# Kernel optimization log

Hardware: AMD Instinct MI355X
Metric: run time of the kernel (lower is better)

## Reference

```python
import jax, jax.numpy as jnp
import numpy as np

STRIDES = (4, 8, 16, 32, 64, 128)
MAPS = (128, 64, 32, 16, 8, 4)
VAR0, VAR1 = 0.1, 0.2
CLS_TH, NMS_TH, FINAL_TH = 0.05, 0.3, 0.5


def _decode_scale(ocls, oreg, stride):
    # ocls: [1,2,H,W], oreg: [1,4,H,W] -> dets [H*W, 5] = (x1,y1,x2,y2,score)
    prob = jax.nn.softmax(ocls, axis=1)[0, 1]          # [H,W] face probability
    H, W = prob.shape
    s = jnp.float32(stride)
    pcx = s / 2 + jnp.arange(W, dtype=jnp.float32)[None, :] * s   # prior center x
    pcy = s / 2 + jnp.arange(H, dtype=jnp.float32)[:, None] * s   # prior center y
    pwh = s * 4.0                                                 # prior w = h = 4*stride
    loc = oreg[0]                                                 # [4,H,W]
    cx = pcx + loc[0] * VAR0 * pwh
    cy = pcy + loc[1] * VAR0 * pwh
    w = pwh * jnp.exp(loc[2] * VAR1)
    h = pwh * jnp.exp(loc[3] * VAR1)
    x1 = cx - w / 2
    y1 = cy - h / 2
    x2 = x1 + w
    y2 = y1 + h
    return jnp.stack([x1.ravel(), y1.ravel(), x2.ravel(), y2.ravel(), prob.ravel()], axis=1)


def _nms_keep(dets, valid):
    # Greedy NMS (torch-style, +1 box convention), fixed trip count, returns keep mask.
    N = dets.shape[0]
    scores = jnp.where(valid, dets[:, 4], -jnp.inf)
    order = jnp.argsort(-scores)            # descending by score, invalid last
    b = dets[order]
    v = valid[order]
    x1, y1, x2, y2 = b[:, 0], b[:, 1], b[:, 2], b[:, 3]
    areas = (x2 - x1 + 1.0) * (y2 - y1 + 1.0)
    pos = jnp.arange(N)

    def body(i, carry):
        sup, keep = carry
        active = jnp.logical_and(jnp.logical_not(sup[i]), v[i])
        keep = keep.at[i].set(active)
        xx1 = jnp.maximum(x1[i], x1)
        yy1 = jnp.maximum(y1[i], y1)
        xx2 = jnp.minimum(x2[i], x2)
        yy2 = jnp.minimum(y2[i], y2)
        w = jnp.maximum(xx2 - xx1 + 1.0, 0.0)
        h = jnp.maximum(yy2 - yy1 + 1.0, 0.0)
        inter = w * h
        iou = inter / (areas[i] + areas - inter)
        sup = sup | (active & (iou > NMS_TH) & (pos > i))
        return sup, keep

    sup0 = jnp.logical_not(v)
    _, keep_sorted = jax.lax.fori_loop(0, N, body, (sup0, jnp.zeros(N, dtype=bool)))
    return jnp.zeros(N, dtype=bool).at[order].set(keep_sorted)


def _forward(ol1, ol2, ol3, ol4, ol5, ol6, ol7, ol8, ol9, ol10, ol11, ol12):
    olist = [ol1, ol2, ol3, ol4, ol5, ol6, ol7, ol8, ol9, ol10, ol11, ol12]
    dets = jnp.concatenate(
        [_decode_scale(olist[2 * i], olist[2 * i + 1], STRIDES[i]) for i in range(6)],
        axis=0)                              # [N,5]
    valid = dets[:, 4] > CLS_TH              # threshold stage (score > 0.05)
    # NMS selection is index logic -> constant w.r.t. differentiation
    keep = _nms_keep(jax.lax.stop_gradient(dets), valid)
    final = keep & (dets[:, 4] > FINAL_TH)   # post-NMS score > 0.5 filter
    # fixed-shape equivalent of gathering kept rows: zero out non-kept rows
    return dets * final[:, None].astype(dets.dtype)


def setup_inputs() -> dict:
    key = jax.random.key(0)
    inp = {}
    for i, hw in enumerate(MAPS):
        kc, kr, key = jax.random.split(key, 3)
        inp[f"ol{2 * i + 1}"] = jax.random.normal(kc, (1, 2, hw, hw), dtype=jnp.float32)
        inp[f"ol{2 * i + 2}"] = jax.random.normal(kr, (1, 4, hw, hw), dtype=jnp.float32)
    return inp


def reference(ol1, ol2, ol3, ol4, ol5, ol6, ol7, ol8, ol9, ol10, ol11, ol12):
    return _forward(ol1, ol2, ol3, ol4, ol5, ol6, ol7, ol8, ol9, ol10, ol11, ol12)
```

## Files before the change

kernel.cpp:

```cpp
#include <hip/hip_runtime.h>
#include <stdint.h>

#define N_TOTAL 21840
#define NA      21888
#define W_MAX   342
#define TOT_ENT 3753792u
#define NMS_TH  0.3f
#define FINAL_TH 0.5f
#define NSLICE  8
#define SCAN_T  768
#define NPUSH   11
#define PLANES  704
#define GRP     4
#define NBAND   7
#define GMAX    86

struct Inputs { const float* cls[6]; const float* reg[6]; };

__device__ __forceinline__ void block_bar() {
  asm volatile("s_waitcnt lgkmcnt(0)\n\ts_barrier" ::: "memory");
}

__device__ __forceinline__ unsigned wbase_u(unsigned w) {
  return 64u * (342u * w - (w * (w - 1u)) / 2u);
}

__global__ void decode_kernel(Inputs in,
                              float* __restrict__ dx1, float* __restrict__ dy1,
                              float* __restrict__ dx2, float* __restrict__ dy2,
                              float* __restrict__ dsc,
                              unsigned long long* __restrict__ ckey,
                              unsigned int* __restrict__ Mc,
                              unsigned int* __restrict__ rank32,
                              unsigned int* __restrict__ wcnt,
                              float* __restrict__ out) {
#pragma clang fp contract(off)
  int gid = blockIdx.x * blockDim.x + threadIdx.x;
  if (gid >= N_TOTAL) return;

  rank32[gid] = 0u;
  wcnt[gid] = 0u;
  if (gid < NA - N_TOTAL) wcnt[N_TOTAL + gid] = 0u;

  int sc, local;
  if      (gid < 16384) { sc = 0; local = gid;         }
  else if (gid < 20480) { sc = 1; local = gid - 16384; }
  else if (gid < 21504) { sc = 2; local = gid - 20480; }
  else if (gid < 21760) { sc = 3; local = gid - 21504; }
  else if (gid < 21824) { sc = 4; local = gid - 21760; }
  else                  { sc = 5; local = gid - 21824; }

  const int Wd     = 128 >> sc;
  const int stride = 4 << sc;
  const int HW     = Wd * Wd;
  const int x = local & (Wd - 1);
  const int y = local >> (7 - sc);

  const float* cls = in.cls[sc];
  const float* reg = in.reg[sc];

  float c0 = cls[local];
  float c1 = cls[HW + local];
  float m  = fmaxf(c0, c1);
  float e0 = expf(c0 - m);
  float e1 = expf(c1 - m);
  float prob = e1 / (e0 + e1);

  float l0 = reg[local];
  float l1 = reg[HW + local];
  float l2 = reg[2 * HW + local];
  float l3 = reg[3 * HW + local];

  float sF  = (float)stride;
  float pcx = 0.5f * sF + (float)x * sF;
  float pcy = 0.5f * sF + (float)y * sF;
  float pwh = sF * 4.0f;

  float cx = pcx + ((l0 * 0.1f) * pwh);
  float cy = pcy + ((l1 * 0.1f) * pwh);
  float w  = pwh * expf(l2 * 0.2f);
  float h  = pwh * expf(l3 * 0.2f);
  float x1 = cx - w * 0.5f;
  float y1 = cy - h * 0.5f;
  float x2 = x1 + w;
  float y2 = y1 + h;

  dx1[gid] = x1; dy1[gid] = y1; dx2[gid] = x2; dy2[gid] = y2; dsc[gid] = prob;

  out[gid * 5 + 0] = 0.0f;
  out[gid * 5 + 1] = 0.0f;
  out[gid * 5 + 2] = 0.0f;
  out[gid * 5 + 3] = 0.0f;
  out[gid * 5 + 4] = 0.0f;

  if (prob > FINAL_TH) {
    unsigned int pos = atomicAdd(Mc, 1u);
    ckey[pos] = ((unsigned long long)__float_as_uint(prob) << 32) |
                (unsigned int)(~(unsigned int)gid);
  }
}

__global__ void __launch_bounds__(256)
rank_kernel(const unsigned long long* __restrict__ ckey,
            const unsigned int* __restrict__ Mc,
            const float* __restrict__ dx1, const float* __restrict__ dy1,
            const float* __restrict__ dx2, const float* __restrict__ dy2,
            float* __restrict__ sx1, float* __restrict__ sy1,
            float* __restrict__ sx2, float* __restrict__ sy2,
            unsigned int* __restrict__ sorig,
            unsigned int* __restrict__ rank32) {
  __shared__ unsigned long long tile[256];
  const unsigned int M = *Mc;
  if (blockIdx.x * 256u >= M) return;
  const int t = (int)threadIdx.x;
  const int p = (int)blockIdx.x * 256 + t;
  unsigned long long mykey = (p < (int)M) ? ckey[p] : 0ull;
  const int S  = (int)((M + NSLICE - 1) / NSLICE);
  const int lo = (int)blockIdx.y * S;
  const int hi = min((int)M, lo + S);
  int partial = 0;
  const int nt = (hi > lo) ? ((hi - lo + 255) >> 8) : 0;
  for (int ti = 0; ti < nt; ++ti) {
    int j = lo + ti * 256 + t;
    tile[t] = (j < hi) ? ckey[j] : 0ull;
    __syncthreads();
#pragma unroll 8
    for (int q = 0; q < 256; ++q) partial += (tile[q] > mykey) ? 1 : 0;
    __syncthreads();
  }
  if (p < (int)M) {
    unsigned int pack = (unsigned int)partial | (1u << 24);
    unsigned int old  = atomicAdd(&rank32[p], pack);
    unsigned int newv = old + pack;
    if ((newv >> 24) == NSLICE) {
      int r = (int)(newv & 0xFFFFFF);
      unsigned int orig = ~(unsigned int)(mykey & 0xffffffffull);
      sx1[r] = dx1[orig];
      sy1[r] = dy1[orig];
      sx2[r] = dx2[orig];
      sy2[r] = dy2[orig];
      sorig[r] = orig;
    }
  }
}

__global__ void __launch_bounds__(1024)
pairs_kernel(const float* __restrict__ sx1, const float* __restrict__ sy1,
             const float* __restrict__ sx2, const float* __restrict__ sy2,
             const unsigned int* __restrict__ Mc,
             unsigned long long* __restrict__ diag,
             unsigned long long* __restrict__ bandT,
             unsigned int* __restrict__ wcnt,
             unsigned short* __restrict__ rlMeta,
             unsigned long long* __restrict__ rlBits) {
#pragma clang fp contract(off)
  const int M = (int)*Mc;
  const int W = (M + 63) >> 6;
  const int rw = (int)blockIdx.y;
  const int cwg = (int)blockIdx.x << 4;
  if (rw >= W || cwg >= W || cwg + 22 < rw) return;

  const int t = (int)threadIdx.x;
  const int g = t >> 6, l = t & 63;
  const int cw = cwg + g;

  __shared__ float cx1[1024], cy1[1024], cx2[1024], cy2[1024], car[1024];
  __shared__ unsigned wvcnt[16], wvbase[16];
  {
    int c = (cw << 6) + l;
    if (cw < W && c < M) {
      float a = sx1[c], b = sy1[c], d = sx2[c], e = sy2[c];
      cx1[t] = a; cy1[t] = b; cx2[t] = d; cy2[t] = e;
      car[t] = (d - a + 1.0f) * (e - b + 1.0f);
    }
  }
  __syncthreads();

  const int rwg = rw >> 2, cg = cw >> 2;
  const bool inW    = (cw < W);
  const bool isDiag = inW && (cw == rw);
  const bool isBand = inW && (cw < rw) && (cg >= rwg - 1);
  const bool isCsr  = inW && (cg >= rwg + 2);
  const bool any    = isDiag || isBand || isCsr;

  const int r = (rw << 6) + l;
  unsigned long long bits = 0ull;
  if (any && r < M) {
    float ax1 = sx1[r], ay1 = sy1[r], ax2 = sx2[r], ay2 = sy2[r];
    float aarea = (ax2 - ax1 + 1.0f) * (ay2 - ay1 + 1.0f);
    const int cmax = min(64, M - (cw << 6));
    const int sb = g << 6;
    for (int cc = 0; cc < cmax; ++cc) {
      float xx1 = fmaxf(ax1, cx1[sb + cc]);
      float yy1 = fmaxf(ay1, cy1[sb + cc]);
      float xx2 = fminf(ax2, cx2[sb + cc]);
      float yy2 = fminf(ay2, cy2[sb + cc]);
      float ww = fmaxf(xx2 - xx1 + 1.0f, 0.0f);
      float hh = fmaxf(yy2 - yy1 + 1.0f, 0.0f);
      float inter = ww * hh;
      float iou = inter / (aarea + car[sb + cc] - inter);
      if (iou > NMS_TH) bits |= (1ull << cc);
    }
  }
  if (isDiag)      diag[r] = bits;
  else if (isBand) bandT[(size_t)(rw - cw - 1) * NA + r] = bits;

  unsigned long long ball = 0ull;
  unsigned myrank = 0u;
  {
    bool mine = isCsr && (bits != 0ull);
    ball = __ballot(mine);
    myrank = (unsigned)__popcll(ball & ((1ull << l) - 1ull));
    if (l == 0) wvcnt[g] = (unsigned)__popcll(ball);
  }
  __syncthreads();
  if (t == 0) {
    unsigned tot = 0u;
    unsigned pre[16];
#pragma unroll
    for (int i = 0; i < 16; ++i) { pre[i] = tot; tot += wvcnt[i]; }
    unsigned base = (tot != 0u) ? atomicAdd(&wcnt[rw], tot) : 0u;
#pragma unroll
    for (int i = 0; i < 16; ++i) wvbase[i] = base + pre[i];
  }
  __syncthreads();
  if (isCsr && bits != 0ull) {
    unsigned slot = wbase_u((unsigned)rw) + wvbase[g] + myrank;
    rlMeta[slot] = (unsigned short)(((unsigned)l << 9) | (unsigned)cw);
    rlBits[slot] = bits;
  }
}

__global__ void __launch_bounds__(SCAN_T)
scan_kernel(const unsigned long long* __restrict__ diag,
            const unsigned long long* __restrict__ bandT,
            const unsigned int* __restrict__ wcnt,
            const unsigned short* __restrict__ rlMeta,
            const unsigned long long* __restrict__ rlBits,
            const unsigned int* __restrict__ sorig,
            const unsigned int* __restrict__ Mc,
            const float* __restrict__ dx1, const float* __restrict__ dy1,
            const float* __restrict__ dx2, const float* __restrict__ dy2,
            const float* __restrict__ dsc,
            float* __restrict__ out) {
  __shared__ unsigned long long sup[W_MAX];
  __shared__ unsigned long long kmls[W_MAX];
  __shared__ unsigned lds_wcnt[W_MAX];
  __shared__ unsigned gdone[GMAX];
  __shared__ volatile unsigned sflag;
  const int t = (int)threadIdx.x;
  const int g = t >> 6, l = t & 63;
  const int M = (int)*Mc;
  const int W = (M + 63) >> 6;
  const int NS = (W + 3) >> 2;

  for (int i = t; i < W_MAX; i += SCAN_T) {
    sup[i] = 0ull; kmls[i] = 0ull; lds_wcnt[i] = wcnt[i];
  }
  for (int i = t; i < GMAX; i += SCAN_T) gdone[i] = 0u;
  if (t == 0) sflag = 0u;
  block_bar();

  if (g == 0) {
    __builtin_amdgcn_s_setprio(1);
    const unsigned long long lowm = (1ull << l) - 1ull;
    unsigned long long dc[4], dn[4];
    unsigned long long bc[4][NBAND], bn[4][NBAND];
    unsigned long long kp[4] = {0ull, 0ull, 0ull, 0ull};
#pragma unroll
    for (int i = 0; i < 4; ++i) {
      int v = i, vc = (v < W) ? v : 0;
      dc[i] = diag[(vc << 6) + l];
#pragma unroll
      for (int d = 1; d <= NBAND; ++d)
        if (d <= i + 4) bc[i][d - 1] = bandT[(size_t)(d - 1) * NA + (vc << 6) + l];
    }
#pragma unroll
    for (int i = 0; i < 4; ++i) {
      int v = 4 + i, vc = (v < W) ? v : 0;
      dn[i] = diag[(vc << 6) + l];
#pragma unroll
      for (int d = 1; d <= NBAND; ++d)
        if (d <= i + 4) bn[i][d - 1] = bandT[(size_t)(d - 1) * NA + (vc << 6) + l];
    }
    for (int s = 0; s < NS; ++s) {
      const int v0 = s << 2;
      unsigned long long accp[4];
#pragma unroll
      for (int i = 0; i < 4; ++i) {
        unsigned long long a = 0ull;
#pragma unroll
        for (int d = 1; d <= NBAND; ++d)
          if (d <= i + 4 && d > i) a |= (bc[i][d - 1] & kp[i - d + 4]);
        accp[i] = a;
      }
      if (s >= 2) {
        while (*(volatile unsigned*)&gdone[s - 2] < (unsigned)NPUSH) {}
        asm volatile("" ::: "memory");
      }
      unsigned long long sv[4];
#pragma unroll
      for (int i = 0; i < 4; ++i)
        sv[i] = (v0 + i < W) ? sup[v0 + i] : 0ull;
      unsigned long long kc[4];
#pragma unroll
      for (int i = 0; i < 4; ++i) {
        const int v = v0 + i;
        unsigned long long kept = 0ull;
        if (v < W) {
          unsigned long long acc = accp[i];
#pragma unroll
          for (int d = 1; d <= 3; ++d)
            if (d <= i) acc |= (bc[i][d - 1] & kc[i - d]);
          unsigned long long incoming = __ballot(acc != 0ull);
          const int n = min(64, M - (v << 6));
          unsigned long long wm = (n >= 64) ? ~0ull : ((1ull << n) - 1ull);
          unsigned long long pend = (~(sv[i] | incoming)) & wm;
          const unsigned long long dv = dc[i] & lowm;
          unsigned long long dead = ~pend, und = pend;
          while (und) {
            unsigned long long bS = __ballot((dv & kept) != 0ull) & und;
            unsigned long long bK = __ballot((dv & ~dead) == 0ull) & und;
            kept |= bK; dead |= bS; und &= ~(bK | bS);
          }
          if (l == i) kmls[v] = kept;
        }
        kc[i] = kept;
      }
      asm volatile("s_waitcnt lgkmcnt(0)" ::: "memory");
      if (l == 0) sflag = (unsigned)(s + 1);
#pragma unroll
      for (int i = 0; i < 4; ++i) kp[i] = kc[i];
#pragma unroll
      for (int i = 0; i < 4; ++i) {
        dc[i] = dn[i];
#pragma unroll
        for (int d = 0; d < NBAND; ++d)
          if (d <= i + 3) bc[i][d] = bn[i][d];
      }
      const int vn = v0 + 8;
#pragma unroll
      for (int i = 0; i < 4; ++i) {
        int v = vn + i, vc = (v < W) ? v : 0;
        dn[i] = diag[(vc << 6) + l];
#pragma unroll
        for (int d = 1; d <= NBAND; ++d)
          if (d <= i + 4) bn[i][d - 1] = bandT[(size_t)(d - 1) * NA + (vc << 6) + l];
      }
    }
    __builtin_amdgcn_s_setprio(0);
  } else {
    const int p = (g - 1) * 64 + l;

#define PUSH_LOAD(mX, bX, gs)                                               \
    {                                                                       \
      _Pragma("unroll")                                                     \
      for (int i = 0; i < 4; ++i) {                                         \
        int v = (gs) * 4 + i;                                               \
        unsigned vc = (v < W) ? (unsigned)v : 0u;                           \
        unsigned base = wbase_u(vc);                                        \
        unsigned i0 = base + (unsigned)p;   if (i0 >= TOT_ENT) i0 = 0u;     \
        unsigned i1 = i0 + (unsigned)PLANES; if (i1 >= TOT_ENT) i1 = 0u;    \
        mX[i][0] = (unsigned)rlMeta[i0]; bX[i][0] = rlBits[i0];             \
        mX[i][1] = (unsigned)rlMeta[i1]; bX[i][1] = rlBits[i1];             \
      }                                                                     \
    }

    unsigned mA[4][2], mB[4][2];
    unsigned long long bA[4][2], bB[4][2];
    PUSH_LOAD(mA, bA, 0)
    PUSH_LOAD(mB, bB, 1)
    for (int s = 0; s < NS; ++s) {
      while (sflag < (unsigned)(s + 1)) __builtin_amdgcn_s_sleep(1);
      asm volatile("" ::: "memory");
#pragma unroll
      for (int i = 0; i < 4; ++i) {
        const int v = (s << 2) + i;
        if (v < W) {
          const unsigned tw = lds_wcnt[v];
          const unsigned long long km = kmls[v];
          if (km != 0ull && tw != 0u) {
            if ((unsigned)p < tw && ((km >> (mA[i][0] >> 9)) & 1ull))
              atomicOr(&sup[mA[i][0] & 511u], bA[i][0]);
            if ((unsigned)p + (unsigned)PLANES < tw &&
                ((km >> (mA[i][1] >> 9)) & 1ull))
              atomicOr(&sup[mA[i][1] & 511u], bA[i][1]);
            if (tw > 2u * (unsigned)PLANES) {
              unsigned base = wbase_u((unsigned)v);
              for (unsigned ii = (unsigned)p + 2u * (unsigned)PLANES;
                   ii < tw; ii += (unsigned)PLANES) {
                unsigned sl = base + ii; if (sl >= TOT_ENT) sl = TOT_ENT - 1u;
                unsigned mm = (unsigned)rlMeta[sl];
                if ((km >> (mm >> 9)) & 1ull)
                  atomicOr(&sup[mm & 511u], rlBits[sl]);
              }
            }
          }
        }
      }
      asm volatile("s_waitcnt lgkmcnt(0)" ::: "memory");
      if (l == 0) atomicAdd(&gdone[s], 1u);
#pragma unroll
      for (int i = 0; i < 4; ++i) {
        mA[i][0] = mB[i][0]; mA[i][1] = mB[i][1];
        bA[i][0] = bB[i][0]; bA[i][1] = bB[i][1];
      }
      PUSH_LOAD(mB, bB, s + 2)
    }
#undef PUSH_LOAD
  }
  block_bar();

  for (int i = t; i < (W << 6); i += SCAN_T) {
    if ((kmls[i >> 6] >> (i & 63)) & 1ull) {
      unsigned int orig = sorig[i];
      out[(size_t)orig * 5 + 0] = dx1[orig];
      out[(size_t)orig * 5 + 1] = dy1[orig];
      out[(size_t)orig * 5 + 2] = dx2[orig];
      out[(size_t)orig * 5 + 3] = dy2[orig];
      out[(size_t)orig * 5 + 4] = dsc[orig];
    }
  }
}

__global__ void __launch_bounds__(1024)
nms_kernel(const float* __restrict__ sx1, const float* __restrict__ sy1,
           const float* __restrict__ sx2, const float* __restrict__ sy2,
           const unsigned int* __restrict__ sorig,
           const unsigned int* __restrict__ Mc,
           unsigned int* __restrict__ keepflag) {
#pragma clang fp contract(off)
  __shared__ unsigned long long sup[W_MAX];
  __shared__ unsigned long long inrow[64];
  __shared__ float wx1[64], wy1[64], wx2[64], wy2[64], warea[64];
  __shared__ unsigned long long keptmask_sh;

  const int t = (int)threadIdx.x;
  const int M = (int)*Mc;
  const int W = (M + 63) >> 6;

  for (int i = t; i < W_MAX; i += 1024) sup[i] = 0ull;
  __syncthreads();

  for (int w = 0; w < W; ++w) {
    const int base = w << 6;
    const int n = min(64, M - base);
    if (t < 64) {
      if (t < n) {
        float a = sx1[base + t], b = sy1[base + t];
        float c = sx2[base + t], d = sy2[base + t];
        wx1[t] = a; wy1[t] = b; wx2[t] = c; wy2[t] = d;
        warea[t] = (c - a + 1.0f) * (d - b + 1.0f);
      }
    } else if (t < 128) {
      inrow[t - 64] = 0ull;
    }
    __syncthreads();
    {
      int r = t & 63, seg = t >> 6;
      unsigned long long bits = 0ull;
      if (r < n) {
        float ax1 = wx1[r], ay1 = wy1[r], ax2 = wx2[r], ay2 = wy2[r];
        float aarea = warea[r];
        for (int c = seg * 4; c < seg * 4 + 4; ++c) {
          if (c > r && c < n) {
            float xx1 = fmaxf(ax1, wx1[c]);
            float yy1 = fmaxf(ay1, wy1[c]);
            float xx2 = fminf(ax2, wx2[c]);
            float yy2 = fminf(ay2, wy2[c]);
            float ww = fmaxf(xx2 - xx1 + 1.0f, 0.0f);
            float hh = fmaxf(yy2 - yy1 + 1.0f, 0.0f);
            float inter = ww * hh;
            float iou = inter / (aarea + warea[c] - inter);
            if (iou > NMS_TH) bits |= (1ull << c);
          }
        }
      }
      if (bits) atomicOr(&inrow[r], bits);
    }
    __syncthreads();
    if (t < 64) {
      unsigned long long wordmask = (n >= 64) ? ~0ull : ((1ull << n) - 1ull);
      unsigned long long pending = (~sup[w]) & wordmask;
      unsigned long long kept = 0ull;
      while (pending) {
        int i = __builtin_ctzll(pending);
        kept |= (1ull << i);
        pending &= ~(inrow[i] | (1ull << i));
      }
      if (t == 0) keptmask_sh = kept;
      if (t < n && ((kept >> t) & 1ull)) keepflag[sorig[base + t]] = 1u;
    }
    __syncthreads();
    unsigned long long km = keptmask_sh;
    if (km) {
      int wid = t >> 6, lane = t & 63;
      for (int jw = w + 1 + wid; (jw << 6) < M; jw += 16) {
        int j = (jw << 6) + lane;
        bool supj = false;
        if (j < M) {
          float jx1 = sx1[j], jy1 = sy1[j], jx2 = sx2[j], jy2 = sy2[j];
          float jarea = (jx2 - jx1 + 1.0f) * (jy2 - jy1 + 1.0f);
          unsigned long long mm = km;
          while (mm) {
            int r = __builtin_ctzll(mm);
            mm &= mm - 1ull;
            float xx1 = fmaxf(wx1[r], jx1);
            float yy1 = fmaxf(wy1[r], jy1);
            float xx2 = fminf(wx2[r], jx2);
            float yy2 = fminf(wy2[r], jy2);
            float ww = fmaxf(xx2 - xx1 + 1.0f, 0.0f);
            float hh = fmaxf(yy2 - yy1 + 1.0f, 0.0f);
            float inter = ww * hh;
            float iou = inter / (warea[r] + jarea - inter);
            if (iou > NMS_TH) { supj = true; break; }
          }
        }
        unsigned long long bal = __ballot(supj);
        if (lane == 0 && bal) atomicOr(&sup[jw], bal);
      }
    }
    __syncthreads();
  }
}

__global__ void output_kernel(const float* __restrict__ dx1, const float* __restrict__ dy1,
                              const float* __restrict__ dx2, const float* __restrict__ dy2,
                              const float* __restrict__ dsc,
                              const unsigned int* __restrict__ keepflag,
                              float* __restrict__ out) {
#pragma clang fp contract(off)
  int gid = blockIdx.x * blockDim.x + threadIdx.x;
  if (gid >= N_TOTAL) return;
  float f = keepflag[gid] ? 1.0f : 0.0f;
  out[gid * 5 + 0] = dx1[gid] * f;
  out[gid * 5 + 1] = dy1[gid] * f;
  out[gid * 5 + 2] = dx2[gid] * f;
  out[gid * 5 + 3] = dy2[gid] * f;
  out[gid * 5 + 4] = dsc[gid] * f;
}

extern "C" void kernel_launch(void* const* d_in, const int* in_sizes, int n_in,
                              void* d_out, int out_size, void* d_ws, size_t ws_size,
                              hipStream_t stream) {
  (void)in_sizes; (void)n_in; (void)out_size;

  Inputs in;
  for (int i = 0; i < 6; ++i) {
    in.cls[i] = (const float*)d_in[2 * i];
    in.reg[i] = (const float*)d_in[2 * i + 1];
  }

  char* ws = (char*)d_ws;
  size_t o = 0;
  float* dx1 = (float*)(ws + o); o += (size_t)NA * 4;
  float* dy1 = (float*)(ws + o); o += (size_t)NA * 4;
  float* dx2 = (float*)(ws + o); o += (size_t)NA * 4;
  float* dy2 = (float*)(ws + o); o += (size_t)NA * 4;
  float* dsc = (float*)(ws + o); o += (size_t)NA * 4;
  unsigned long long* ckey = (unsigned long long*)(ws + o); o += (size_t)NA * 8;
  float* sx1 = (float*)(ws + o); o += (size_t)NA * 4;
  float* sy1 = (float*)(ws + o); o += (size_t)NA * 4;
  float* sx2 = (float*)(ws + o); o += (size_t)NA * 4;
  float* sy2 = (float*)(ws + o); o += (size_t)NA * 4;
  unsigned int* sorig = (unsigned int*)(ws + o); o += (size_t)NA * 4;
  unsigned int* keepflag = (unsigned int*)(ws + o); o += (size_t)NA * 4;
  unsigned int* rank32 = (unsigned int*)(ws + o); o += (size_t)NA * 4;
  unsigned int* wcnt = (unsigned int*)(ws + o); o += (size_t)NA * 4;
  unsigned int* Mc = (unsigned int*)(ws + o); o += 64;
  o = (o + 511) & ~(size_t)511;
  unsigned long long* diag = (unsigned long long*)(ws + o); o += (size_t)NA * 8;
  unsigned long long* bandT = (unsigned long long*)(ws + o); o += (size_t)NBAND * NA * 8;
  unsigned long long* rlBits = (unsigned long long*)(ws + o); o += (size_t)TOT_ENT * 8;
  unsigned short* rlMeta = (unsigned short*)(ws + o); o += (size_t)TOT_ENT * 2;
  size_t need = o;
  const bool fast = (need <= ws_size);

  const int nb = (N_TOTAL + 255) / 256;

  if (fast) {
    (void)hipMemsetAsync((void*)Mc, 0, 64, stream);
    decode_kernel<<<nb, 256, 0, stream>>>(in, dx1, dy1, dx2, dy2, dsc, ckey, Mc,
                                          rank32, wcnt, (float*)d_out);
    rank_kernel<<<dim3(nb, NSLICE), 256, 0, stream>>>(ckey, Mc, dx1, dy1, dx2, dy2,
                                                      sx1, sy1, sx2, sy2, sorig,
                                                      rank32);
    pairs_kernel<<<dim3(22, W_MAX), 1024, 0, stream>>>(sx1, sy1, sx2, sy2, Mc,
                                                       diag, bandT, wcnt, rlMeta, rlBits);
    scan_kernel<<<1, SCAN_T, 0, stream>>>(diag, bandT, wcnt, rlMeta, rlBits, sorig, Mc,
                                          dx1, dy1, dx2, dy2, dsc, (float*)d_out);
  } else {
    (void)hipMemsetAsync((void*)keepflag, 0, (size_t)NA * 12 + 64, stream);
    decode_kernel<<<nb, 256, 0, stream>>>(in, dx1, dy1, dx2, dy2, dsc, ckey, Mc,
                                          rank32, wcnt, (float*)d_out);
    rank_kernel<<<dim3(nb, NSLICE), 256, 0, stream>>>(ckey, Mc, dx1, dy1, dx2, dy2,
                                                      sx1, sy1, sx2, sy2, sorig,
                                                      rank32);
    nms_kernel<<<1, 1024, 0, stream>>>(sx1, sy1, sx2, sy2, sorig, Mc, keepflag);
    output_kernel<<<nb, 256, 0, stream>>>(dx1, dy1, dx2, dy2, dsc, keepflag,
                                          (float*)d_out);
  }
}
```

Before: 261.7 us.

## Shrink scan group to three words, double-buffer scan registers, deepen push prefetch

Changes the sequential NMS scan to resolve word-groups of three 64-box words instead of four, which shrinks the band of precomputed suppression words from seven to five and adjusts the pairs kernel's classification to match. The scan wave's register double buffering becomes a ping-pong unrolled pair of steps, which removes the per-step register copies. The push waves now prefetch four plane entries per word instead of two. The intent is a shorter critical path per scan step and fewer serial global loads in the push phase, at the cost of more scan steps and more register pressure. Padded diag and band arrays (NA2) avoid out-of-range reads when prefetching past W.

```diff
diff --git a/kernel.cpp b/kernel.cpp
--- a/kernel.cpp
+++ b/kernel.cpp
@@ -4,6 +4,7 @@
 #define N_TOTAL 21840
 #define NA      21888
 #define W_MAX   342
+#define NA2     22528
 #define TOT_ENT 3753792u
 #define NMS_TH  0.3f
 #define FINAL_TH 0.5f
@@ -11,9 +12,10 @@
 #define SCAN_T  768
 #define NPUSH   11
 #define PLANES  704
-#define GRP     4
-#define NBAND   7
-#define GMAX    86
+#define GRP     3
+#define NBAND   5
+#define GMAX    114
+#define DEPTH   4
 
 struct Inputs { const float* cls[6]; const float* reg[6]; };
 
@@ -158,7 +160,7 @@
   const int W = (M + 63) >> 6;
   const int rw = (int)blockIdx.y;
   const int cwg = (int)blockIdx.x << 4;
-  if (rw >= W || cwg >= W || cwg + 22 < rw) return;
+  if (rw >= W || cwg >= W || cwg + 20 < rw) return;
 
   const int t = (int)threadIdx.x;
   const int g = t >> 6, l = t & 63;
@@ -176,7 +178,7 @@
   }
   __syncthreads();
 
-  const int rwg = rw >> 2, cg = cw >> 2;
+  const int rwg = rw / 3, cg = cw / 3;
   const bool inW    = (cw < W);
   const bool isDiag = inW && (cw == rw);
   const bool isBand = inW && (cw < rw) && (cg >= rwg - 1);
@@ -203,7 +205,7 @@
     }
   }
   if (isDiag)      diag[r] = bits;
-  else if (isBand) bandT[(size_t)(rw - cw - 1) * NA + r] = bits;
+  else if (isBand) bandT[(size_t)(rw - cw - 1) * NA2 + r] = bits;
 
   unsigned long long ball = 0ull;
   unsigned myrank = 0u;
@@ -252,7 +254,7 @@
   const int g = t >> 6, l = t & 63;
   const int M = (int)*Mc;
   const int W = (M + 63) >> 6;
-  const int NS = (W + 3) >> 2;
+  const int NS = (W + 2) / 3;
 
   for (int i = t; i < W_MAX; i += SCAN_T) {
     sup[i] = 0ull; kmls[i] = 0ull; lds_wcnt[i] = wcnt[i];
@@ -264,150 +266,147 @@
   if (g == 0) {
     __builtin_amdgcn_s_setprio(1);
     const unsigned long long lowm = (1ull << l) - 1ull;
-    unsigned long long dc[4], dn[4];
-    unsigned long long bc[4][NBAND], bn[4][NBAND];
-    unsigned long long kp[4] = {0ull, 0ull, 0ull, 0ull};
-#pragma unroll
-    for (int i = 0; i < 4; ++i) {
-      int v = i, vc = (v < W) ? v : 0;
-      dc[i] = diag[(vc << 6) + l];
-#pragma unroll
-      for (int d = 1; d <= NBAND; ++d)
-        if (d <= i + 4) bc[i][d - 1] = bandT[(size_t)(d - 1) * NA + (vc << 6) + l];
-    }
-#pragma unroll
-    for (int i = 0; i < 4; ++i) {
-      int v = 4 + i, vc = (v < W) ? v : 0;
-      dn[i] = diag[(vc << 6) + l];
-#pragma unroll
-      for (int d = 1; d <= NBAND; ++d)
-        if (d <= i + 4) bn[i][d - 1] = bandT[(size_t)(d - 1) * NA + (vc << 6) + l];
-    }
-    for (int s = 0; s < NS; ++s) {
-      const int v0 = s << 2;
-      unsigned long long accp[4];
-#pragma unroll
-      for (int i = 0; i < 4; ++i) {
-        unsigned long long a = 0ull;
-#pragma unroll
-        for (int d = 1; d <= NBAND; ++d)
-          if (d <= i + 4 && d > i) a |= (bc[i][d - 1] & kp[i - d + 4]);
-        accp[i] = a;
-      }
-      if (s >= 2) {
-        while (*(volatile unsigned*)&gdone[s - 2] < (unsigned)NPUSH) {}
-        asm volatile("" ::: "memory");
-      }
-      unsigned long long sv[4];
-#pragma unroll
-      for (int i = 0; i < 4; ++i)
-        sv[i] = (v0 + i < W) ? sup[v0 + i] : 0ull;
-      unsigned long long kc[4];
-#pragma unroll
-      for (int i = 0; i < 4; ++i) {
-        const int v = v0 + i;
-        unsigned long long kept = 0ull;
-        if (v < W) {
-          unsigned long long acc = accp[i];
-#pragma unroll
-          for (int d = 1; d <= 3; ++d)
-            if (d <= i) acc |= (bc[i][d - 1] & kc[i - d]);
-          unsigned long long incoming = __ballot(acc != 0ull);
-          const int n = min(64, M - (v << 6));
-          unsigned long long wm = (n >= 64) ? ~0ull : ((1ull << n) - 1ull);
-          unsigned long long pend = (~(sv[i] | incoming)) & wm;
-          const unsigned long long dv = dc[i] & lowm;
-          unsigned long long dead = ~pend, und = pend;
-          while (und) {
-            unsigned long long bS = __ballot((dv & kept) != 0ull) & und;
-            unsigned long long bK = __ballot((dv & ~dead) == 0ull) & und;
-            kept |= bK; dead |= bS; und &= ~(bK | bS);
-          }
-          if (l == i) kmls[v] = kept;
-        }
-        kc[i] = kept;
-      }
-      asm volatile("s_waitcnt lgkmcnt(0)" ::: "memory");
-      if (l == 0) sflag = (unsigned)(s + 1);
-#pragma unroll
-      for (int i = 0; i < 4; ++i) kp[i] = kc[i];
-#pragma unroll
-      for (int i = 0; i < 4; ++i) {
-        dc[i] = dn[i];
-#pragma unroll
-        for (int d = 0; d < NBAND; ++d)
-          if (d <= i + 3) bc[i][d] = bn[i][d];
-      }
-      const int vn = v0 + 8;
-#pragma unroll
-      for (int i = 0; i < 4; ++i) {
-        int v = vn + i, vc = (v < W) ? v : 0;
-        dn[i] = diag[(vc << 6) + l];
-#pragma unroll
-        for (int d = 1; d <= NBAND; ++d)
-          if (d <= i + 4) bn[i][d - 1] = bandT[(size_t)(d - 1) * NA + (vc << 6) + l];
-      }
-    }
+    unsigned long long dA[3], dB[3];
+    unsigned long long bA_[3][NBAND], bB_[3][NBAND];
+    unsigned long long kp[3] = {0ull, 0ull, 0ull};
+
+#define SCAN_PROLOAD(DC_, BC_, GS_)                                         \
+    { _Pragma("unroll")                                                     \
+      for (int i = 0; i < 3; ++i) {                                         \
+        const int v_ = (GS_) * 3 + i;                                       \
+        DC_[i] = diag[(v_ << 6) + l];                                       \
+        _Pragma("unroll")                                                   \
+        for (int d = 1; d <= NBAND; ++d)                                    \
+          if (d <= i + 3)                                                   \
+            BC_[i][d - 1] = bandT[(size_t)(d - 1) * NA2 + (v_ << 6) + l];   \
+      } }
+
+    SCAN_PROLOAD(dA, bA_, 0)
+    SCAN_PROLOAD(dB, bB_, 1)
+
+#define SCAN_STEP(DC_, BC_, S_)                                             \
+    { const int s_ = (S_);                                                  \
+      const int v0_ = s_ * 3;                                               \
+      unsigned long long accp[3];                                           \
+      _Pragma("unroll")                                                     \
+      for (int i = 0; i < 3; ++i) {                                         \
+        unsigned long long a = 0ull;                                        \
+        _Pragma("unroll")                                                   \
+        for (int d = 1; d <= NBAND; ++d)                                    \
+          if (d <= i + 3 && d > i) a |= (BC_[i][d - 1] & kp[i - d + 3]);    \
+        accp[i] = a;                                                        \
+      }                                                                     \
+      if (s_ >= 2) {                                                        \
+        while (*(volatile unsigned*)&gdone[s_ - 2] < (unsigned)NPUSH) {}    \
+        asm volatile("" ::: "memory");                                      \
+      }                                                                     \
+      unsigned long long sv[3];                                             \
+      _Pragma("unroll")                                                     \
+      for (int i = 0; i < 3; ++i)                                           \
+        sv[i] = (v0_ + i < W) ? sup[v0_ + i] : 0ull;                        \
+      unsigned long long kc[3];                                             \
+      _Pragma("unroll")                                                     \
+      for (int i = 0; i < 3; ++i) {                                         \
+        const int v_ = v0_ + i;                                             \
+        unsigned long long kept = 0ull;                                     \
+        if (v_ < W) {                                                       \
+          unsigned long long acc = accp[i];                                 \
+          _Pragma("unroll")                                                 \
+          for (int d = 1; d <= 2; ++d)                                      \
+            if (d <= i) acc |= (BC_[i][d - 1] & kc[i - d]);                 \
+          unsigned long long incoming = __ballot(acc != 0ull);              \
+          const int n_ = min(64, M - (v_ << 6));                            \
+          unsigned long long wm =                                           \
+              (n_ >= 64) ? ~0ull : ((1ull << n_) - 1ull);                   \
+          unsigned long long pend = (~(sv[i] | incoming)) & wm;             \
+          const unsigned long long dv = DC_[i] & lowm;                      \
+          unsigned long long dead = ~pend, und = pend;                      \
+          while (und) {                                                     \
+            unsigned long long bS = __ballot((dv & kept) != 0ull) & und;    \
+            unsigned long long bK = __ballot((dv & ~dead) == 0ull) & und;   \
+            kept |= bK; dead |= bS; und &= ~(bK | bS);                      \
+          }                                                                 \
+          if (l == i) kmls[v_] = kept;                                      \
+        }                                                                   \
+        kc[i] = kept;                                                       \
+      }                                                                     \
+      asm volatile("s_waitcnt lgkmcnt(0)" ::: "memory");                    \
+      if (l == 0) sflag = (unsigned)(s_ + 1);                               \
+      SCAN_PROLOAD(DC_, BC_, s_ + 2)    \
+      _Pragma("unroll")                                                     \
+      for (int i = 0; i < 3; ++i) kp[i] = kc[i];                            \
+    }
+
+    for (int s = 0; s < NS; s += 2) {
+      SCAN_STEP(dA, bA_, s)
+      if (s + 1 < NS) SCAN_STEP(dB, bB_, s + 1)
+    }
+#undef SCAN_STEP
+#undef SCAN_PROLOAD
     __builtin_amdgcn_s_setprio(0);
   } else {
     const int p = (g - 1) * 64 + l;
-
-#define PUSH_LOAD(mX, bX, gs)                                               \
-    {                                                                       \
+    unsigned mA[3][DEPTH], mB[3][DEPTH];
+    unsigned long long bA[3][DEPTH], bB[3][DEPTH];
+
+#define PUSH_LOAD4(MX_, BX_, GS_)                                           \
+    { _Pragma("unroll")                                                     \
+      for (int i = 0; i < 3; ++i) {                                         \
+        int v_ = (GS_) * 3 + i;                                             \
+        unsigned vc_ = (v_ < W) ? (unsigned)v_ : 0u;                        \
+        unsigned base_ = wbase_u(vc_) + (unsigned)p;                        \
+        _Pragma("unroll")                                                   \
+        for (int k = 0; k < DEPTH; ++k) {                                   \
+          unsigned ii_ = base_ + (unsigned)(k * PLANES);                    \
+          if (ii_ >= TOT_ENT) ii_ = 0u;                                     \
+          MX_[i][k] = (unsigned)rlMeta[ii_]; BX_[i][k] = rlBits[ii_];       \
+        }                                                                   \
+      } }
+
+#define PUSH_STEP(MC_, BC2_, S_)                                            \
+    { const int s_ = (S_);                                                  \
+      while (sflag < (unsigned)(s_ + 1)) __builtin_amdgcn_s_sleep(1);       \
+      asm volatile("" ::: "memory");                                        \
       _Pragma("unroll")                                                     \
-      for (int i = 0; i < 4; ++i) {                                         \
-        int v = (gs) * 4 + i;                                               \
-        unsigned vc = (v < W) ? (unsigned)v : 0u;                           \
-        unsigned base = wbase_u(vc);                                        \
-        unsigned i0 = base + (unsigned)p;   if (i0 >= TOT_ENT) i0 = 0u;     \
-        unsigned i1 = i0 + (unsigned)PLANES; if (i1 >= TOT_ENT) i1 = 0u;    \
-        mX[i][0] = (unsigned)rlMeta[i0]; bX[i][0] = rlBits[i0];             \
-        mX[i][1] = (unsigned)rlMeta[i1]; bX[i][1] = rlBits[i1];             \
+      for (int i = 0; i < 3; ++i) {                                         \
+        const int v_ = s_ * 3 + i;                                          \
+        if (v_ < W) {                                                       \
+          const unsigned tw_ = lds_wcnt[v_];                                \
+          const unsigned long long km_ = kmls[v_];                          \
+          if (km_ != 0ull && tw_ != 0u) {                                   \
+            _Pragma("unroll")                                               \
+            for (int k = 0; k < DEPTH; ++k) {                               \
+              if ((unsigned)p + (unsigned)(k * PLANES) < tw_ &&             \
+                  ((km_ >> (MC_[i][k] >> 9)) & 1ull))                       \
+                atomicOr(&sup[MC_[i][k] & 511u], BC2_[i][k]);               \
+            }                                                               \
+            if (tw_ > (unsigned)(DEPTH * PLANES)) {        \
+              unsigned base_ = wbase_u((unsigned)v_);                       \
+              for (unsigned ii_ = (unsigned)p + (unsigned)(DEPTH * PLANES); \
+                   ii_ < tw_; ii_ += (unsigned)PLANES) {                    \
+                unsigned sl_ = base_ + ii_;                                 \
+                if (sl_ >= TOT_ENT) sl_ = TOT_ENT - 1u;                     \
+                unsigned mm_ = (unsigned)rlMeta[sl_];                       \
+                if ((km_ >> (mm_ >> 9)) & 1ull)                             \
+                  atomicOr(&sup[mm_ & 511u], rlBits[sl_]);                  \
+              }                                                             \
+            }                                                               \
+          }                                                                 \
+        }                                                                   \
       }                                                                     \
-    }
-
-    unsigned mA[4][2], mB[4][2];
-    unsigned long long bA[4][2], bB[4][2];
-    PUSH_LOAD(mA, bA, 0)
-    PUSH_LOAD(mB, bB, 1)
-    for (int s = 0; s < NS; ++s) {
-      while (sflag < (unsigned)(s + 1)) __builtin_amdgcn_s_sleep(1);
-      asm volatile("" ::: "memory");
-#pragma unroll
-      for (int i = 0; i < 4; ++i) {
-        const int v = (s << 2) + i;
-        if (v < W) {
-          const unsigned tw = lds_wcnt[v];
-          const unsigned long long km = kmls[v];
-          if (km != 0ull && tw != 0u) {
-            if ((unsigned)p < tw && ((km >> (mA[i][0] >> 9)) & 1ull))
-              atomicOr(&sup[mA[i][0] & 511u], bA[i][0]);
-            if ((unsigned)p + (unsigned)PLANES < tw &&
-                ((km >> (mA[i][1] >> 9)) & 1ull))
-              atomicOr(&sup[mA[i][1] & 511u], bA[i][1]);
-            if (tw > 2u * (unsigned)PLANES) {
-              unsigned base = wbase_u((unsigned)v);
-              for (unsigned ii = (unsigned)p + 2u * (unsigned)PLANES;
-                   ii < tw; ii += (unsigned)PLANES) {
-                unsigned sl = base + ii; if (sl >= TOT_ENT) sl = TOT_ENT - 1u;
-                unsigned mm = (unsigned)rlMeta[sl];
-                if ((km >> (mm >> 9)) & 1ull)
-                  atomicOr(&sup[mm & 511u], rlBits[sl]);
-              }
-            }
-          }
-        }
-      }
-      asm volatile("s_waitcnt lgkmcnt(0)" ::: "memory");
-      if (l == 0) atomicAdd(&gdone[s], 1u);
-#pragma unroll
-      for (int i = 0; i < 4; ++i) {
-        mA[i][0] = mB[i][0]; mA[i][1] = mB[i][1];
-        bA[i][0] = bB[i][0]; bA[i][1] = bB[i][1];
-      }
-      PUSH_LOAD(mB, bB, s + 2)
-    }
-#undef PUSH_LOAD
+      asm volatile("s_waitcnt lgkmcnt(0)" ::: "memory");                    \
+      if (l == 0) atomicAdd(&gdone[s_], 1u);                                \
+      PUSH_LOAD4(MC_, BC2_, s_ + 2)                                         \
+    }
+
+    PUSH_LOAD4(mA, bA, 0)
+    PUSH_LOAD4(mB, bB, 1)
+    for (int s = 0; s < NS; s += 2) {
+      PUSH_STEP(mA, bA, s)
+      if (s + 1 < NS) PUSH_STEP(mB, bB, s + 1)
+    }
+#undef PUSH_STEP
+#undef PUSH_LOAD4
   }
   block_bar();
 
@@ -569,8 +568,8 @@
   unsigned int* wcnt = (unsigned int*)(ws + o); o += (size_t)NA * 4;
   unsigned int* Mc = (unsigned int*)(ws + o); o += 64;
   o = (o + 511) & ~(size_t)511;
-  unsigned long long* diag = (unsigned long long*)(ws + o); o += (size_t)NA * 8;
-  unsigned long long* bandT = (unsigned long long*)(ws + o); o += (size_t)NBAND * NA * 8;
+  unsigned long long* diag = (unsigned long long*)(ws + o); o += (size_t)NA2 * 8;
+  unsigned long long* bandT = (unsigned long long*)(ws + o); o += (size_t)NBAND * NA2 * 8;
   unsigned long long* rlBits = (unsigned long long*)(ws + o); o += (size_t)TOT_ENT * 8;
   unsigned short* rlMeta = (unsigned short*)(ws + o); o += (size_t)TOT_ENT * 2;
   size_t need = o;
```

After: 297.1 us. 13.5% more time.

## Offload cross-step band suppression to helper waves, shrink scan critical path

Applied to the files above, without the earlier changes.

Moves the band-overlap suppression from the previous 4-word step out of the serial scan wave into four helper wavefronts. Each helper computes an incoming-suppression ballot for one word of the next step and publishes it through shared memory, with an hdone counter for handshaking. The scan wave then keeps only the within-step band registers, which cuts its register load and per-step work. The push waves drop from 11 to 7 and prefetch 3 planes instead of 2 to make up for it. This adds another cross-wave spin-wait per step and lowers push parallelism, which may lengthen the push stage.

```diff
diff --git a/kernel.cpp b/kernel.cpp
--- a/kernel.cpp
+++ b/kernel.cpp
@@ -9,8 +9,9 @@
 #define FINAL_TH 0.5f
 #define NSLICE  8
 #define SCAN_T  768
-#define NPUSH   11
-#define PLANES  704
+#define NPUSHF  7
+#define PLANESF 448
+#define DEPTH   3
 #define GRP     4
 #define NBAND   7
 #define GMAX    86
@@ -247,6 +248,8 @@
   __shared__ unsigned long long kmls[W_MAX];
   __shared__ unsigned lds_wcnt[W_MAX];
   __shared__ unsigned gdone[GMAX];
+  __shared__ unsigned hdone[GMAX];
+  __shared__ unsigned long long incArr[4];
   __shared__ volatile unsigned sflag;
   const int t = (int)threadIdx.x;
   const int g = t >> 6, l = t & 63;
@@ -257,7 +260,8 @@
   for (int i = t; i < W_MAX; i += SCAN_T) {
     sup[i] = 0ull; kmls[i] = 0ull; lds_wcnt[i] = wcnt[i];
   }
-  for (int i = t; i < GMAX; i += SCAN_T) gdone[i] = 0u;
+  for (int i = t; i < GMAX; i += SCAN_T) { gdone[i] = 0u; hdone[i] = 0u; }
+  if (t < 4) incArr[t] = 0ull;
   if (t == 0) sflag = 0u;
   block_bar();
 
@@ -265,37 +269,34 @@
     __builtin_amdgcn_s_setprio(1);
     const unsigned long long lowm = (1ull << l) - 1ull;
     unsigned long long dc[4], dn[4];
-    unsigned long long bc[4][NBAND], bn[4][NBAND];
-    unsigned long long kp[4] = {0ull, 0ull, 0ull, 0ull};
-#pragma unroll
-    for (int i = 0; i < 4; ++i) {
-      int v = i, vc = (v < W) ? v : 0;
-      dc[i] = diag[(vc << 6) + l];
-#pragma unroll
-      for (int d = 1; d <= NBAND; ++d)
-        if (d <= i + 4) bc[i][d - 1] = bandT[(size_t)(d - 1) * NA + (vc << 6) + l];
-    }
-#pragma unroll
-    for (int i = 0; i < 4; ++i) {
-      int v = 4 + i, vc = (v < W) ? v : 0;
-      dn[i] = diag[(vc << 6) + l];
-#pragma unroll
-      for (int d = 1; d <= NBAND; ++d)
-        if (d <= i + 4) bn[i][d - 1] = bandT[(size_t)(d - 1) * NA + (vc << 6) + l];
-    }
+    unsigned long long bc[6], bn[6];
+
+#define SC_LOAD(DD, BB, gs)                                                 \
+    { _Pragma("unroll")                                                     \
+      for (int i = 0; i < 4; ++i) {                                         \
+        int v = (gs) * 4 + i; unsigned vc = (v < W) ? (unsigned)v : 0u;     \
+        DD[i] = diag[(vc << 6) + l];                                        \
+      }                                                                     \
+      _Pragma("unroll")                                                     \
+      for (int i = 1; i < 4; ++i) {                                         \
+        int v = (gs) * 4 + i; unsigned vc = (v < W) ? (unsigned)v : 0u;     \
+        _Pragma("unroll")                                                   \
+        for (int d = 1; d <= 3; ++d)                                        \
+          if (d <= i)                                                       \
+            BB[i * (i - 1) / 2 + (d - 1)] =                                 \
+                bandT[(size_t)(d - 1) * NA + (vc << 6) + l];                \
+      } }
+
+    SC_LOAD(dc, bc, 0)
+    SC_LOAD(dn, bn, 1)
     for (int s = 0; s < NS; ++s) {
       const int v0 = s << 2;
-      unsigned long long accp[4];
-#pragma unroll
-      for (int i = 0; i < 4; ++i) {
-        unsigned long long a = 0ull;
-#pragma unroll
-        for (int d = 1; d <= NBAND; ++d)
-          if (d <= i + 4 && d > i) a |= (bc[i][d - 1] & kp[i - d + 4]);
-        accp[i] = a;
+      if (s >= 1) {
+        while (*(volatile unsigned*)&hdone[s] < 4u) {}
+        asm volatile("" ::: "memory");
       }
       if (s >= 2) {
-        while (*(volatile unsigned*)&gdone[s - 2] < (unsigned)NPUSH) {}
+        while (*(volatile unsigned*)&gdone[s - 2] < (unsigned)NPUSHF) {}
         asm volatile("" ::: "memory");
       }
       unsigned long long sv[4];
@@ -308,11 +309,12 @@
         const int v = v0 + i;
         unsigned long long kept = 0ull;
         if (v < W) {
-          unsigned long long acc = accp[i];
+          unsigned long long acc = 0ull;
 #pragma unroll
           for (int d = 1; d <= 3; ++d)
-            if (d <= i) acc |= (bc[i][d - 1] & kc[i - d]);
+            if (d <= i) acc |= (bc[i * (i - 1) / 2 + (d - 1)] & kc[i - d]);
           unsigned long long incoming = __ballot(acc != 0ull);
+          if (s >= 1) incoming |= incArr[i];
           const int n = min(64, M - (v << 6));
           unsigned long long wm = (n >= 64) ? ~0ull : ((1ull << n) - 1ull);
           unsigned long long pend = (~(sv[i] | incoming)) & wm;
@@ -330,44 +332,65 @@
       asm volatile("s_waitcnt lgkmcnt(0)" ::: "memory");
       if (l == 0) sflag = (unsigned)(s + 1);
 #pragma unroll
-      for (int i = 0; i < 4; ++i) kp[i] = kc[i];
-#pragma unroll
-      for (int i = 0; i < 4; ++i) {
-        dc[i] = dn[i];
-#pragma unroll
-        for (int d = 0; d < NBAND; ++d)
-          if (d <= i + 3) bc[i][d] = bn[i][d];
-      }
-      const int vn = v0 + 8;
-#pragma unroll
-      for (int i = 0; i < 4; ++i) {
-        int v = vn + i, vc = (v < W) ? v : 0;
-        dn[i] = diag[(vc << 6) + l];
-#pragma unroll
-        for (int d = 1; d <= NBAND; ++d)
-          if (d <= i + 4) bn[i][d - 1] = bandT[(size_t)(d - 1) * NA + (vc << 6) + l];
-      }
-    }
+      for (int i = 0; i < 4; ++i) dc[i] = dn[i];
+#pragma unroll
+      for (int i = 0; i < 6; ++i) bc[i] = bn[i];
+      SC_LOAD(dn, bn, s + 2)
+    }
+#undef SC_LOAD
     __builtin_amdgcn_s_setprio(0);
+  } else if (g <= 4) {
+    const int i = g - 1;
+    unsigned long long hA[4], hB[4];
+#define H_LOAD(HX, gs)                                                      \
+    { _Pragma("unroll")                                                     \
+      for (int dd = 0; dd < 4; ++dd) {                                      \
+        int v = (gs) * 4 + i; unsigned vc = (v < W) ? (unsigned)v : 0u;     \
+        HX[dd] = bandT[(size_t)(i + dd) * NA + (vc << 6) + l];              \
+      } }
+    H_LOAD(hA, 0)
+    H_LOAD(hB, 1)
+    for (int s = 0; s < NS; ++s) {
+      while (sflag < (unsigned)s) __builtin_amdgcn_s_sleep(1);
+      asm volatile("" ::: "memory");
+      unsigned long long acc = 0ull;
+      if (s >= 1) {
+        const int u0 = (s - 1) * 4;
+#pragma unroll
+        for (int dd = 0; dd < 4; ++dd) {
+          int u = u0 + 3 - dd;
+          unsigned long long km = (u < W) ? kmls[u] : 0ull;
+          acc |= (hA[dd] & km);
+        }
+      }
+      unsigned long long inc = __ballot(acc != 0ull);
+      if (l == 0) incArr[i] = inc;
+      asm volatile("s_waitcnt lgkmcnt(0)" ::: "memory");
+      if (l == 0) atomicAdd(&hdone[s], 1u);
+#pragma unroll
+      for (int dd = 0; dd < 4; ++dd) hA[dd] = hB[dd];
+      H_LOAD(hB, s + 2)
+    }
+#undef H_LOAD
   } else {
-    const int p = (g - 1) * 64 + l;
+    const int p = (g - 5) * 64 + l;
 
 #define PUSH_LOAD(mX, bX, gs)                                               \
-    {                                                                       \
-      _Pragma("unroll")                                                     \
+    { _Pragma("unroll")                                                     \
       for (int i = 0; i < 4; ++i) {                                         \
         int v = (gs) * 4 + i;                                               \
         unsigned vc = (v < W) ? (unsigned)v : 0u;                           \
-        unsigned base = wbase_u(vc);                                        \
-        unsigned i0 = base + (unsigned)p;   if (i0 >= TOT_ENT) i0 = 0u;     \
-        unsigned i1 = i0 + (unsigned)PLANES; if (i1 >= TOT_ENT) i1 = 0u;    \
-        mX[i][0] = (unsigned)rlMeta[i0]; bX[i][0] = rlBits[i0];             \
-        mX[i][1] = (unsigned)rlMeta[i1]; bX[i][1] = rlBits[i1];             \
-      }                                                                     \
-    }
-
-    unsigned mA[4][2], mB[4][2];
-    unsigned long long bA[4][2], bB[4][2];
+        unsigned base = wbase_u(vc) + (unsigned)p;                          \
+        _Pragma("unroll")                                                   \
+        for (int k = 0; k < DEPTH; ++k) {                                   \
+          unsigned ii = base + (unsigned)(k * PLANESF);                     \
+          if (ii >= TOT_ENT) ii = 0u;                                       \
+          mX[i][k] = (unsigned)rlMeta[ii]; bX[i][k] = rlBits[ii];           \
+        }                                                                   \
+      } }
+
+    unsigned mA[4][DEPTH], mB[4][DEPTH];
+    unsigned long long bA[4][DEPTH], bB[4][DEPTH];
     PUSH_LOAD(mA, bA, 0)
     PUSH_LOAD(mB, bB, 1)
     for (int s = 0; s < NS; ++s) {
@@ -380,15 +403,16 @@
           const unsigned tw = lds_wcnt[v];
           const unsigned long long km = kmls[v];
           if (km != 0ull && tw != 0u) {
-            if ((unsigned)p < tw && ((km >> (mA[i][0] >> 9)) & 1ull))
-              atomicOr(&sup[mA[i][0] & 511u], bA[i][0]);
-            if ((unsigned)p + (unsigned)PLANES < tw &&
-                ((km >> (mA[i][1] >> 9)) & 1ull))
-              atomicOr(&sup[mA[i][1] & 511u], bA[i][1]);
-            if (tw > 2u * (unsigned)PLANES) {
+#pragma unroll
+            for (int k = 0; k < DEPTH; ++k) {
+              if ((unsigned)p + (unsigned)(k * PLANESF) < tw &&
+                  ((km >> (mA[i][k] >> 9)) & 1ull))
+                atomicOr(&sup[mA[i][k] & 511u], bA[i][k]);
+            }
+            if (tw > (unsigned)(DEPTH * PLANESF)) {
               unsigned base = wbase_u((unsigned)v);
-              for (unsigned ii = (unsigned)p + 2u * (unsigned)PLANES;
-                   ii < tw; ii += (unsigned)PLANES) {
+              for (unsigned ii = (unsigned)p + (unsigned)(DEPTH * PLANESF);
+                   ii < tw; ii += (unsigned)PLANESF) {
                 unsigned sl = base + ii; if (sl >= TOT_ENT) sl = TOT_ENT - 1u;
                 unsigned mm = (unsigned)rlMeta[sl];
                 if ((km >> (mm >> 9)) & 1ull)
@@ -401,10 +425,9 @@
       asm volatile("s_waitcnt lgkmcnt(0)" ::: "memory");
       if (l == 0) atomicAdd(&gdone[s], 1u);
 #pragma unroll
-      for (int i = 0; i < 4; ++i) {
-        mA[i][0] = mB[i][0]; mA[i][1] = mB[i][1];
-        bA[i][0] = bB[i][0]; bA[i][1] = bB[i][1];
-      }
+      for (int i = 0; i < 4; ++i)
+#pragma unroll
+        for (int k = 0; k < DEPTH; ++k) { mA[i][k] = mB[i][k]; bA[i][k] = bB[i][k]; }
       PUSH_LOAD(mB, bB, s + 2)
     }
 #undef PUSH_LOAD
```

New measurement: 266.9 us. No clear change (+2.0%).

## Stage serial-wave diag/band rows into LDS ring via async global_load_lds

Applied to the files above, without the earlier changes.

The serial scan wave used to double-buffer diagonal and band bitmask rows in registers (two sets of 26 u64 values per lane). It now issues async global-to-LDS loads (global_load_lds, 16 bytes per lane) into a two-slot LDS ring, waits with vmcnt(13) for the current stage, and reads the operands from LDS. The aim is to cut register pressure and the register shuffling on the latency-critical serial path. In exchange it adds LDS reads inside the inner dependency chain and about 26 KB of extra shared memory, and it relies on vmcnt accounting for correctness. Refilling a ring slot right after it is read also risks a write-after-read race if the LDS reads have not completed.

```diff
diff --git a/kernel.cpp b/kernel.cpp
--- a/kernel.cpp
+++ b/kernel.cpp
@@ -14,6 +14,8 @@
 #define GRP     4
 #define NBAND   7
 #define GMAX    86
+#define NROWS   26
+#define NSTG    13
 
 struct Inputs { const float* cls[6]; const float* reg[6]; };
 
@@ -23,6 +25,25 @@
 
 __device__ __forceinline__ unsigned wbase_u(unsigned w) {
   return 64u * (342u * w - (w * (w - 1u)) / 2u);
+}
+
+#define BROW(i, d) ((i) == 0 ? 3 + (d) : (i) == 1 ? 7 + (d) \
+                    : (i) == 2 ? 12 + (d) : 18 + (d))
+
+__device__ __forceinline__ const unsigned long long*
+row_gbase(int r, int gs, int W,
+          const unsigned long long* diag, const unsigned long long* bandT) {
+  if (r < 4) {
+    int v = gs * 4 + r; unsigned vc = (v < W) ? (unsigned)v : 0u;
+    return diag + ((size_t)vc << 6);
+  }
+  int i, d;
+  if      (r < 8)  { i = 0; d = r - 3;  }
+  else if (r < 13) { i = 1; d = r - 7;  }
+  else if (r < 19) { i = 2; d = r - 12; }
+  else             { i = 3; d = r - 18; }
+  int v = gs * 4 + i; unsigned vc = (v < W) ? (unsigned)v : 0u;
+  return bandT + (size_t)(d - 1) * NA + ((size_t)vc << 6);
 }
 
 __global__ void decode_kernel(Inputs in,
@@ -245,6 +266,7 @@
             float* __restrict__ out) {
   __shared__ unsigned long long sup[W_MAX];
   __shared__ unsigned long long kmls[W_MAX];
+  __shared__ unsigned long long ring[2][NROWS * 64];
   __shared__ unsigned lds_wcnt[W_MAX];
   __shared__ unsigned gdone[GMAX];
   __shared__ volatile unsigned sflag;
@@ -264,39 +286,40 @@
   if (g == 0) {
     __builtin_amdgcn_s_setprio(1);
     const unsigned long long lowm = (1ull << l) - 1ull;
-    unsigned long long dc[4], dn[4];
-    unsigned long long bc[4][NBAND], bn[4][NBAND];
     unsigned long long kp[4] = {0ull, 0ull, 0ull, 0ull};
-#pragma unroll
-    for (int i = 0; i < 4; ++i) {
-      int v = i, vc = (v < W) ? v : 0;
-      dc[i] = diag[(vc << 6) + l];
-#pragma unroll
-      for (int d = 1; d <= NBAND; ++d)
-        if (d <= i + 4) bc[i][d - 1] = bandT[(size_t)(d - 1) * NA + (vc << 6) + l];
-    }
-#pragma unroll
-    for (int i = 0; i < 4; ++i) {
-      int v = 4 + i, vc = (v < W) ? v : 0;
-      dn[i] = diag[(vc << 6) + l];
-#pragma unroll
-      for (int d = 1; d <= NBAND; ++d)
-        if (d <= i + 4) bn[i][d - 1] = bandT[(size_t)(d - 1) * NA + (vc << 6) + l];
-    }
+
+#define STAGE(sl, gs)                                                       \
+    { _Pragma("unroll")                                                     \
+      for (int j = 0; j < NSTG; ++j) {                                      \
+        const unsigned long long* b0 = row_gbase(2 * j,     (gs), W, diag, bandT); \
+        const unsigned long long* b1 = row_gbase(2 * j + 1, (gs), W, diag, bandT); \
+        const char* gb = (const char*)((l < 32) ? b0 : b1)                  \
+                         + (size_t)(l & 31) * 16;                           \
+        char* lb = (char*)&ring[(sl)][0] + (size_t)j * 1024;                \
+        __builtin_amdgcn_global_load_lds(                                   \
+            (const __attribute__((address_space(1))) void*)gb,              \
+            (__attribute__((address_space(3))) void*)lb, 16, 0, 0);         \
+      } }
+
+    STAGE(0, 0)
+    STAGE(1, 1)
     for (int s = 0; s < NS; ++s) {
       const int v0 = s << 2;
-      unsigned long long accp[4];
-#pragma unroll
-      for (int i = 0; i < 4; ++i) {
-        unsigned long long a = 0ull;
-#pragma unroll
-        for (int d = 1; d <= NBAND; ++d)
-          if (d <= i + 4 && d > i) a |= (bc[i][d - 1] & kp[i - d + 4]);
-        accp[i] = a;
-      }
+      const int cur = s & 1;
       if (s >= 2) {
         while (*(volatile unsigned*)&gdone[s - 2] < (unsigned)NPUSH) {}
         asm volatile("" ::: "memory");
+      }
+      asm volatile("s_waitcnt vmcnt(13)" ::: "memory");
+      unsigned long long accp[4];
+#pragma unroll
+      for (int i = 0; i < 4; ++i) {
+        unsigned long long a = 0ull;
+#pragma unroll
+        for (int d = 1; d <= NBAND; ++d)
+          if (d <= i + 4 && d > i)
+            a |= (ring[cur][BROW(i, d) * 64 + l] & kp[i - d + 4]);
+        accp[i] = a;
       }
       unsigned long long sv[4];
 #pragma unroll
@@ -311,12 +334,13 @@
           unsigned long long acc = accp[i];
 #pragma unroll
           for (int d = 1; d <= 3; ++d)
-            if (d <= i) acc |= (bc[i][d - 1] & kc[i - d]);
+            if (d <= i)
+              acc |= (ring[cur][BROW(i, d) * 64 + l] & kc[i - d]);
           unsigned long long incoming = __ballot(acc != 0ull);
           const int n = min(64, M - (v << 6));
           unsigned long long wm = (n >= 64) ? ~0ull : ((1ull << n) - 1ull);
           unsigned long long pend = (~(sv[i] | incoming)) & wm;
-          const unsigned long long dv = dc[i] & lowm;
+          const unsigned long long dv = ring[cur][i * 64 + l] & lowm;
           unsigned long long dead = ~pend, und = pend;
           while (und) {
             unsigned long long bS = __ballot((dv & kept) != 0ull) & und;
@@ -331,23 +355,9 @@
       if (l == 0) sflag = (unsigned)(s + 1);
 #pragma unroll
       for (int i = 0; i < 4; ++i) kp[i] = kc[i];
-#pragma unroll
-      for (int i = 0; i < 4; ++i) {
-        dc[i] = dn[i];
-#pragma unroll
-        for (int d = 0; d < NBAND; ++d)
-          if (d <= i + 3) bc[i][d] = bn[i][d];
-      }
-      const int vn = v0 + 8;
-#pragma unroll
-      for (int i = 0; i < 4; ++i) {
-        int v = vn + i, vc = (v < W) ? v : 0;
-        dn[i] = diag[(vc << 6) + l];
-#pragma unroll
-        for (int d = 1; d <= NBAND; ++d)
-          if (d <= i + 4) bn[i][d - 1] = bandT[(size_t)(d - 1) * NA + (vc << 6) + l];
-      }
-    }
+      STAGE(cur, s + 2)
+    }
+#undef STAGE
     __builtin_amdgcn_s_setprio(0);
   } else {
     const int p = (g - 1) * 64 + l;
```

Result: slower. 270.6 us (+3.4%).
